# Kernel tuning notes

Hardware: AMD Instinct MI355X
Metric: run time of the kernel (lower is better)

The kernel has to match this reference:

```python
import jax, jax.numpy as jnp
import numpy as np

B, N, M, D = 8, 512, 64, 128
H = 64  # mlp_hidden_dim


def setup_inputs() -> dict:
    key = jax.random.key(0)
    ks = jax.random.split(key, 10)
    op_emb = jax.random.normal(ks[0], (B, N, D), dtype=jnp.float32)
    machine_emb = jax.random.normal(ks[1], (B, M, D), dtype=jnp.float32)
    edge_emb = jax.random.normal(ks[2], (B, N, M, D), dtype=jnp.float32)
    action_mask = jax.random.randint(ks[3], (B, N, M), 0, 2) > 0
    s1 = 1.0 / np.sqrt(3 * D)
    s2 = 1.0 / np.sqrt(H)
    W1 = jax.random.uniform(ks[4], (3 * D, H), jnp.float32, -s1, s1)
    b1 = jax.random.uniform(ks[5], (H,), jnp.float32, -s1, s1)
    W2 = jax.random.uniform(ks[6], (H, H), jnp.float32, -s2, s2)
    b2 = jax.random.uniform(ks[7], (H,), jnp.float32, -s2, s2)
    W3 = jax.random.uniform(ks[8], (H, 1), jnp.float32, -s2, s2)
    b3 = jax.random.uniform(ks[9], (1,), jnp.float32, -s2, s2)
    return {"op_emb": op_emb, "machine_emb": machine_emb, "edge_emb": edge_emb,
            "action_mask": action_mask,
            "W1": W1, "b1": b1, "W2": W2, "b2": b2, "W3": W3, "b3": b3}


def reference(op_emb, machine_emb, edge_emb, action_mask, W1, b1, W2, b2, W3, b3):
    # Split first linear over the three concat chunks to avoid materializing
    # the (B,N,M,3D) concat tensor (same math as cat -> Linear).
    Wo, Wm, We = W1[:D], W1[D:2 * D], W1[2 * D:]
    h = (jnp.einsum('bnd,dh->bnh', op_emb, Wo)[:, :, None, :]
         + jnp.einsum('bmd,dh->bmh', machine_emb, Wm)[:, None, :, :]
         + jnp.einsum('bnmd,dh->bnmh', edge_emb, We) + b1)  # (B,N,M,H)
    h = jax.nn.relu(h)
    h = jax.nn.relu(h @ W2 + b2)
    scores = (h @ W3 + b3)[..., 0]  # (B,N,M)
    scores = jnp.where(action_mask, scores, -jnp.inf)
    return jax.nn.log_softmax(scores.reshape(B, N * M), axis=-1)
```

## Files before the change

### kernel.cpp

```cpp
#include <hip/hip_runtime.h>
#include <math.h>

#define Bb 8
#define Nn 512
#define Mm 64
#define Dd 128
#define Hh 64
#define Gg 4
#define NEG_BIG (-1.0e30f)

typedef __bf16 bf16x8 __attribute__((ext_vector_type(8)));
typedef float  f32x4  __attribute__((ext_vector_type(4)));

#define WS_WEB   0u
#define WS_W2B   16384u
#define WS_CWS   24576u
#define WS_AOP   155648u
#define WS_SCORE 1204224u

__global__ __launch_bounds__(256) void wprep_kernel(
    const float* __restrict__ W1, const float* __restrict__ W2, char* __restrict__ ws)
{
    __bf16* WeB = (__bf16*)(ws + WS_WEB);
    __bf16* W2B = (__bf16*)(ws + WS_W2B);
    int idx = blockIdx.x * 256 + threadIdx.x;
    if (idx < 8192) {
        int fid = idx >> 9, rem = idx & 511;
        int lane = rem >> 3, j = rem & 7;
        int t = fid >> 2, ks = fid & 3;
        int q = lane >> 4, ln = lane & 15;
        int d = ks * 32 + q * 8 + j;
        int h = t * 16 + ln;
        WeB[idx] = (__bf16)W1[(size_t)(2 * Dd + d) * Hh + h];
    } else if (idx < 12288) {
        int i2 = idx - 8192;
        int fid = i2 >> 9, rem = i2 & 511;
        int lane = rem >> 3, j = rem & 7;
        int t = fid >> 1, ks = fid & 1;
        int q = lane >> 4, ln = lane & 15;
        int k = ks * 32 + q * 8 + j;
        int h = t * 16 + ln;
        W2B[i2] = (__bf16)W2[(size_t)k * Hh + h];
    }
}

__global__ __launch_bounds__(64) void proj_kernel(
    const float* __restrict__ op_emb, const float* __restrict__ machine_emb,
    const float* __restrict__ W1, const float* __restrict__ b1, char* __restrict__ ws)
{
    float* Cws = (float*)(ws + WS_CWS);
    float* Aop = (float*)(ws + WS_AOP);
    const int bid = blockIdx.x;
    const int h = threadIdx.x;
    if (bid < Bb * Mm) {
        const float* mg = machine_emb + (size_t)bid * Dd;
        const float* Wm = W1 + (size_t)Dd * Hh;
        float acc = b1[h];
#pragma unroll 8
        for (int d = 0; d < Dd; ++d) acc = fmaf(mg[d], Wm[d * Hh + h], acc);
        Cws[(size_t)bid * Hh + h] = acc;
    } else {
        const int bn = bid - Bb * Mm;
        const float* og = op_emb + (size_t)bn * Dd;
        float acc = 0.f;
#pragma unroll 8
        for (int d = 0; d < Dd; ++d) acc = fmaf(og[d], W1[d * Hh + h], acc);
        Aop[(size_t)bn * Hh + h] = acc;
    }
}

__global__ __launch_bounds__(256, 3) void main_kernel(
    const float* __restrict__ edge_emb, const int* __restrict__ mask,
    const float* __restrict__ b2, const float* __restrict__ W3,
    const float* __restrict__ b3, char* __restrict__ ws)
{
    __shared__ __bf16 sWeB[8192];
    __shared__ __bf16 sW2B[4096];
    __shared__ __bf16 sH1[Mm * 72];

    const float* Cws = (const float*)(ws + WS_CWS);
    const float* Aop = (const float*)(ws + WS_AOP);
    float* scores    = (float*)(ws + WS_SCORE);

    const int tid  = threadIdx.x;
    const int lane = tid & 63;
    const int w    = tid >> 6;
    const int q    = lane >> 4;
    const int ln   = lane & 15;
    const int bn0  = blockIdx.x * Gg;
    const int b    = bn0 >> 9;
    const int mrow = w * 16 + ln;

    {
        const float4* s1 = (const float4*)(ws + WS_WEB);
        float4* d1 = (float4*)sWeB;
        for (int i = tid; i < 1024; i += 256) d1[i] = s1[i];
        const float4* s2 = (const float4*)(ws + WS_W2B);
        float4* d2 = (float4*)sW2B;
        for (int i = tid; i < 512; i += 256) d2[i] = s2[i];
    }

    float cv[16];
#pragma unroll
    for (int t = 0; t < 4; ++t)
#pragma unroll
        for (int r = 0; r < 4; ++r)
            cv[t * 4 + r] = Cws[((size_t)b * Mm + w * 16 + q * 4 + r) * Hh + t * 16 + ln];
    float b2v[4], w3v[4];
#pragma unroll
    for (int t = 0; t < 4; ++t) { b2v[t] = b2[t * 16 + ln]; w3v[t] = W3[t * 16 + ln]; }
    const float bias3 = b3[0];

    float4 raw[8]; float aopv[4]; int4 mk = {0, 0, 0, 0};
    {
        const float* Eg = edge_emb + (size_t)bn0 * (Mm * Dd) + mrow * Dd + q * 8;
#pragma unroll
        for (int ks = 0; ks < 4; ++ks) {
            raw[2 * ks]     = *(const float4*)&Eg[ks * 32];
            raw[2 * ks + 1] = *(const float4*)&Eg[ks * 32 + 4];
        }
#pragma unroll
        for (int t = 0; t < 4; ++t) aopv[t] = Aop[(size_t)bn0 * Hh + t * 16 + ln];
        if (ln == 0) mk = *(const int4*)&mask[(size_t)bn0 * Mm + w * 16 + q * 4];
    }

    __syncthreads();

#pragma unroll
    for (int g = 0; g < Gg; ++g) {
        const int bn = bn0 + g;

        float4 nraw[8] = {};
        float  naop[4] = {};
        int4   nmk = {0, 0, 0, 0};
        if (g + 1 < Gg) {
            const float* Eg = edge_emb + (size_t)(bn + 1) * (Mm * Dd) + mrow * Dd + q * 8;
#pragma unroll
            for (int ks = 0; ks < 4; ++ks) {
                nraw[2 * ks]     = *(const float4*)&Eg[ks * 32];
                nraw[2 * ks + 1] = *(const float4*)&Eg[ks * 32 + 4];
            }
#pragma unroll
            for (int t = 0; t < 4; ++t) naop[t] = Aop[(size_t)(bn + 1) * Hh + t * 16 + ln];
            if (ln == 0) nmk = *(const int4*)&mask[(size_t)(bn + 1) * Mm + w * 16 + q * 4];
        }

        bf16x8 af[4];
#pragma unroll
        for (int ks = 0; ks < 4; ++ks) {
            float4 lo = raw[2 * ks], hi = raw[2 * ks + 1];
            bf16x8 a;
            a[0] = (__bf16)lo.x; a[1] = (__bf16)lo.y; a[2] = (__bf16)lo.z; a[3] = (__bf16)lo.w;
            a[4] = (__bf16)hi.x; a[5] = (__bf16)hi.y; a[6] = (__bf16)hi.z; a[7] = (__bf16)hi.w;
            af[ks] = a;
        }

        f32x4 acc[4];
#pragma unroll
        for (int t = 0; t < 4; ++t) acc[t] = (f32x4){0.f, 0.f, 0.f, 0.f};
#pragma unroll
        for (int t = 0; t < 4; ++t)
#pragma unroll
            for (int ks = 0; ks < 4; ++ks) {
                bf16x8 bfr = *(const bf16x8*)&sWeB[((t * 4 + ks) * 64 + lane) * 8];
                acc[t] = __builtin_amdgcn_mfma_f32_16x16x32_bf16(af[ks], bfr, acc[t], 0, 0, 0);
            }

#pragma unroll
        for (int t = 0; t < 4; ++t) {
            float av = aopv[t];
#pragma unroll
            for (int r = 0; r < 4; ++r) {
                float v = fmaxf(acc[t][r] + av + cv[t * 4 + r], 0.f);
                sH1[(w * 16 + q * 4 + r) * 72 + t * 16 + ln] = (__bf16)v;
            }
        }

        bf16x8 a2[2];
#pragma unroll
        for (int ks = 0; ks < 2; ++ks)
            a2[ks] = *(const bf16x8*)&sH1[(w * 16 + ln) * 72 + ks * 32 + q * 8];
        f32x4 c2[4];
#pragma unroll
        for (int t = 0; t < 4; ++t) c2[t] = (f32x4){0.f, 0.f, 0.f, 0.f};
#pragma unroll
        for (int t = 0; t < 4; ++t)
#pragma unroll
            for (int ks = 0; ks < 2; ++ks) {
                bf16x8 bfr = *(const bf16x8*)&sW2B[((t * 2 + ks) * 64 + lane) * 8];
                c2[t] = __builtin_amdgcn_mfma_f32_16x16x32_bf16(a2[ks], bfr, c2[t], 0, 0, 0);
            }

        float p[4] = {0.f, 0.f, 0.f, 0.f};
#pragma unroll
        for (int t = 0; t < 4; ++t)
#pragma unroll
            for (int r = 0; r < 4; ++r)
                p[r] += fmaxf(c2[t][r] + b2v[t], 0.f) * w3v[t];
#pragma unroll
        for (int r = 0; r < 4; ++r) {
            p[r] += __shfl_xor(p[r], 1, 64);
            p[r] += __shfl_xor(p[r], 2, 64);
            p[r] += __shfl_xor(p[r], 4, 64);
            p[r] += __shfl_xor(p[r], 8, 64);
        }
        if (ln == 0) {
            float4 o;
            o.x = mk.x ? (p[0] + bias3) : NEG_BIG;
            o.y = mk.y ? (p[1] + bias3) : NEG_BIG;
            o.z = mk.z ? (p[2] + bias3) : NEG_BIG;
            o.w = mk.w ? (p[3] + bias3) : NEG_BIG;
            *(float4*)&scores[(size_t)bn * Mm + w * 16 + q * 4] = o;
        }

#pragma unroll
        for (int i = 0; i < 8; ++i) raw[i] = nraw[i];
#pragma unroll
        for (int t = 0; t < 4; ++t) aopv[t] = naop[t];
        mk = nmk;
    }
}

__global__ __launch_bounds__(1024) void lsm_kernel(
    const char* __restrict__ ws, float* __restrict__ out)
{
    const float* s = (const float*)(ws + WS_SCORE) + (size_t)blockIdx.x * (Nn * Mm);
    __shared__ float redA[16];
    __shared__ float redB[16];
    const int tid = threadIdx.x;

    float lm = -INFINITY;
    for (int i = tid; i < Nn * Mm; i += 1024) lm = fmaxf(lm, s[i]);
#pragma unroll
    for (int off = 32; off > 0; off >>= 1) lm = fmaxf(lm, __shfl_xor(lm, off, 64));
    if ((tid & 63) == 0) redA[tid >> 6] = lm;
    __syncthreads();
    float gm = redA[0];
#pragma unroll
    for (int k = 1; k < 16; ++k) gm = fmaxf(gm, redA[k]);

    float ls = 0.f;
    for (int i = tid; i < Nn * Mm; i += 1024) ls += expf(s[i] - gm);
#pragma unroll
    for (int off = 32; off > 0; off >>= 1) ls += __shfl_xor(ls, off, 64);
    if ((tid & 63) == 0) redB[tid >> 6] = ls;
    __syncthreads();
    float gs = 0.f;
#pragma unroll
    for (int k = 0; k < 16; ++k) gs += redB[k];

    const float cc = gm + logf(gs);
    for (int i = tid; i < Nn * Mm; i += 1024)
        out[(size_t)blockIdx.x * (Nn * Mm) + i] = s[i] - cc;
}

extern "C" void kernel_launch(void* const* d_in, const int* in_sizes, int n_in,
                              void* d_out, int out_size, void* d_ws, size_t ws_size,
                              hipStream_t stream)
{
    const float* op_emb      = (const float*)d_in[0];
    const float* machine_emb = (const float*)d_in[1];
    const float* edge_emb    = (const float*)d_in[2];
    const int*   mask        = (const int*)  d_in[3];
    const float* W1 = (const float*)d_in[4];
    const float* b1 = (const float*)d_in[5];
    const float* W2 = (const float*)d_in[6];
    const float* b2 = (const float*)d_in[7];
    const float* W3 = (const float*)d_in[8];
    const float* b3 = (const float*)d_in[9];
    char* ws = (char*)d_ws;

    wprep_kernel<<<48, 256, 0, stream>>>(W1, W2, ws);
    proj_kernel<<<Bb * Mm + Bb * Nn, 64, 0, stream>>>(op_emb, machine_emb, W1, b1, ws);
    main_kernel<<<(Bb * Nn) / Gg, 256, 0, stream>>>(edge_emb, mask, b2, W3, b3, ws);
    lsm_kernel<<<Bb, 1024, 0, stream>>>(ws, (float*)d_out);
}
```

Measured before the change: 244.4 us.

## Split log-softmax into parallel partial, combine and apply kernels; stage biases in LDS

The single 8-block log-softmax kernel is replaced by three kernels: a 512-block pass that computes a per-chunk max and sum-exp, an 8-block combine, and a vectorised elementwise apply. This spreads the reduction across far more CUs than the old 8-block launch. The main kernel now stages the per-batch machine projection, op projection and mask in shared memory and seeds the MFMA accumulators with the bias sum. It also streamlines the prefetch registers. The cost is two extra kernel launches and more LDS per block, which may lower occupancy in the main kernel.

Result: faster. 238.5 us (-2.4%).

```diff
diff --git a/kernel.cpp b/kernel.cpp
--- a/kernel.cpp
+++ b/kernel.cpp
@@ -17,6 +17,8 @@
 #define WS_CWS   24576u
 #define WS_AOP   155648u
 #define WS_SCORE 1204224u
+#define WS_PART  2252800u
+#define WS_CC    2256896u
 
 __global__ __launch_bounds__(256) void wprep_kernel(
     const float* __restrict__ W1, const float* __restrict__ W2, char* __restrict__ ws)
@@ -76,11 +78,12 @@
 {
     __shared__ __bf16 sWeB[8192];
     __shared__ __bf16 sW2B[4096];
+    __shared__ float  sCws[Mm * Hh];
     __shared__ __bf16 sH1[Mm * 72];
-
-    const float* Cws = (const float*)(ws + WS_CWS);
-    const float* Aop = (const float*)(ws + WS_AOP);
-    float* scores    = (float*)(ws + WS_SCORE);
+    __shared__ float  sAop[Gg * Hh];
+    __shared__ int    sMask[Gg * Mm];
+
+    float* scores = (float*)(ws + WS_SCORE);
 
     const int tid  = threadIdx.x;
     const int lane = tid & 63;
@@ -98,30 +101,24 @@
         const float4* s2 = (const float4*)(ws + WS_W2B);
         float4* d2 = (float4*)sW2B;
         for (int i = tid; i < 512; i += 256) d2[i] = s2[i];
-    }
-
-    float cv[16];
-#pragma unroll
-    for (int t = 0; t < 4; ++t)
-#pragma unroll
-        for (int r = 0; r < 4; ++r)
-            cv[t * 4 + r] = Cws[((size_t)b * Mm + w * 16 + q * 4 + r) * Hh + t * 16 + ln];
+        const float4* s3 = (const float4*)(ws + WS_CWS) + (size_t)b * (Mm * Hh / 4);
+        float4* d3 = (float4*)sCws;
+        for (int i = tid; i < 1024; i += 256) d3[i] = s3[i];
+        sAop[tid] = ((const float*)(ws + WS_AOP))[(size_t)bn0 * Hh + tid];
+        sMask[tid] = mask[(size_t)bn0 * Mm + tid];
+    }
+
     float b2v[4], w3v[4];
 #pragma unroll
     for (int t = 0; t < 4; ++t) { b2v[t] = b2[t * 16 + ln]; w3v[t] = W3[t * 16 + ln]; }
     const float bias3 = b3[0];
 
-    float4 raw[8]; float aopv[4]; int4 mk = {0, 0, 0, 0};
-    {
-        const float* Eg = edge_emb + (size_t)bn0 * (Mm * Dd) + mrow * Dd + q * 8;
-#pragma unroll
-        for (int ks = 0; ks < 4; ++ks) {
-            raw[2 * ks]     = *(const float4*)&Eg[ks * 32];
-            raw[2 * ks + 1] = *(const float4*)&Eg[ks * 32 + 4];
-        }
-#pragma unroll
-        for (int t = 0; t < 4; ++t) aopv[t] = Aop[(size_t)bn0 * Hh + t * 16 + ln];
-        if (ln == 0) mk = *(const int4*)&mask[(size_t)bn0 * Mm + w * 16 + q * 4];
+    const float* Eg0 = edge_emb + (size_t)bn0 * (Mm * Dd) + mrow * Dd + q * 8;
+    float4 raw[8];
+#pragma unroll
+    for (int ks = 0; ks < 4; ++ks) {
+        raw[2 * ks]     = *(const float4*)&Eg0[ks * 32];
+        raw[2 * ks + 1] = *(const float4*)&Eg0[ks * 32 + 4];
     }
 
     __syncthreads();
@@ -129,21 +126,6 @@
 #pragma unroll
     for (int g = 0; g < Gg; ++g) {
         const int bn = bn0 + g;
-
-        float4 nraw[8] = {};
-        float  naop[4] = {};
-        int4   nmk = {0, 0, 0, 0};
-        if (g + 1 < Gg) {
-            const float* Eg = edge_emb + (size_t)(bn + 1) * (Mm * Dd) + mrow * Dd + q * 8;
-#pragma unroll
-            for (int ks = 0; ks < 4; ++ks) {
-                nraw[2 * ks]     = *(const float4*)&Eg[ks * 32];
-                nraw[2 * ks + 1] = *(const float4*)&Eg[ks * 32 + 4];
-            }
-#pragma unroll
-            for (int t = 0; t < 4; ++t) naop[t] = Aop[(size_t)(bn + 1) * Hh + t * 16 + ln];
-            if (ln == 0) nmk = *(const int4*)&mask[(size_t)(bn + 1) * Mm + w * 16 + q * 4];
-        }
 
         bf16x8 af[4];
 #pragma unroll
@@ -154,10 +136,24 @@
             a[4] = (__bf16)hi.x; a[5] = (__bf16)hi.y; a[6] = (__bf16)hi.z; a[7] = (__bf16)hi.w;
             af[ks] = a;
         }
+        if (g + 1 < Gg) {
+            const float* Eg = edge_emb + (size_t)(bn + 1) * (Mm * Dd) + mrow * Dd + q * 8;
+#pragma unroll
+            for (int ks = 0; ks < 4; ++ks) {
+                raw[2 * ks]     = *(const float4*)&Eg[ks * 32];
+                raw[2 * ks + 1] = *(const float4*)&Eg[ks * 32 + 4];
+            }
+        }
 
         f32x4 acc[4];
 #pragma unroll
-        for (int t = 0; t < 4; ++t) acc[t] = (f32x4){0.f, 0.f, 0.f, 0.f};
+        for (int t = 0; t < 4; ++t) {
+            float av = sAop[g * Hh + t * 16 + ln];
+#pragma unroll
+            for (int r = 0; r < 4; ++r)
+                acc[t][r] = av + sCws[(w * 16 + q * 4 + r) * Hh + t * 16 + ln];
+        }
+
 #pragma unroll
         for (int t = 0; t < 4; ++t)
 #pragma unroll
@@ -167,14 +163,11 @@
             }
 
 #pragma unroll
-        for (int t = 0; t < 4; ++t) {
-            float av = aopv[t];
-#pragma unroll
-            for (int r = 0; r < 4; ++r) {
-                float v = fmaxf(acc[t][r] + av + cv[t * 4 + r], 0.f);
-                sH1[(w * 16 + q * 4 + r) * 72 + t * 16 + ln] = (__bf16)v;
-            }
-        }
+        for (int t = 0; t < 4; ++t)
+#pragma unroll
+            for (int r = 0; r < 4; ++r)
+                sH1[(w * 16 + q * 4 + r) * 72 + t * 16 + ln] =
+                    (__bf16)fmaxf(acc[t][r], 0.f);
 
         bf16x8 a2[2];
 #pragma unroll
@@ -205,53 +198,70 @@
             p[r] += __shfl_xor(p[r], 8, 64);
         }
         if (ln == 0) {
+            int m0 = w * 16 + q * 4;
             float4 o;
-            o.x = mk.x ? (p[0] + bias3) : NEG_BIG;
-            o.y = mk.y ? (p[1] + bias3) : NEG_BIG;
-            o.z = mk.z ? (p[2] + bias3) : NEG_BIG;
-            o.w = mk.w ? (p[3] + bias3) : NEG_BIG;
-            *(float4*)&scores[(size_t)bn * Mm + w * 16 + q * 4] = o;
-        }
-
-#pragma unroll
-        for (int i = 0; i < 8; ++i) raw[i] = nraw[i];
-#pragma unroll
-        for (int t = 0; t < 4; ++t) aopv[t] = naop[t];
-        mk = nmk;
-    }
-}
-
-__global__ __launch_bounds__(1024) void lsm_kernel(
+            o.x = sMask[g * Mm + m0 + 0] ? (p[0] + bias3) : NEG_BIG;
+            o.y = sMask[g * Mm + m0 + 1] ? (p[1] + bias3) : NEG_BIG;
+            o.z = sMask[g * Mm + m0 + 2] ? (p[2] + bias3) : NEG_BIG;
+            o.w = sMask[g * Mm + m0 + 3] ? (p[3] + bias3) : NEG_BIG;
+            *(float4*)&scores[(size_t)bn * Mm + m0] = o;
+        }
+    }
+}
+
+__global__ __launch_bounds__(256) void lsm_part_kernel(char* __restrict__ ws)
+{
+    const float* s = (const float*)(ws + WS_SCORE);
+    float* part = (float*)(ws + WS_PART);
+    __shared__ float sm[4], ss[4];
+    const int c = blockIdx.x;
+    const int tid = threadIdx.x;
+    const int lane = tid & 63, wv = tid >> 6;
+
+    float2 v = *(const float2*)&s[(size_t)c * 512 + tid * 2];
+    float m = fmaxf(v.x, v.y);
+#pragma unroll
+    for (int off = 1; off < 64; off <<= 1) m = fmaxf(m, __shfl_xor(m, off, 64));
+    if (lane == 0) sm[wv] = m;
+    __syncthreads();
+    float gm = fmaxf(fmaxf(sm[0], sm[1]), fmaxf(sm[2], sm[3]));
+
+    float e = expf(v.x - gm) + expf(v.y - gm);
+#pragma unroll
+    for (int off = 1; off < 64; off <<= 1) e += __shfl_xor(e, off, 64);
+    if (lane == 0) ss[wv] = e;
+    __syncthreads();
+    if (tid == 0) {
+        float2 o; o.x = gm; o.y = ss[0] + ss[1] + ss[2] + ss[3];
+        *(float2*)&part[c * 2] = o;
+    }
+}
+
+__global__ __launch_bounds__(64) void lsm_comb_kernel(char* __restrict__ ws)
+{
+    const float* part = (const float*)(ws + WS_PART);
+    float* cc = (float*)(ws + WS_CC);
+    const int b = blockIdx.x, t = threadIdx.x;
+    float2 p = *(const float2*)&part[(b * 64 + t) * 2];
+    float gm = p.x;
+#pragma unroll
+    for (int off = 1; off < 64; off <<= 1) gm = fmaxf(gm, __shfl_xor(gm, off, 64));
+    float l = p.y * expf(p.x - gm);
+#pragma unroll
+    for (int off = 1; off < 64; off <<= 1) l += __shfl_xor(l, off, 64);
+    if (t == 0) cc[b] = gm + logf(l);
+}
+
+__global__ __launch_bounds__(256) void lsm_apply_kernel(
     const char* __restrict__ ws, float* __restrict__ out)
 {
-    const float* s = (const float*)(ws + WS_SCORE) + (size_t)blockIdx.x * (Nn * Mm);
-    __shared__ float redA[16];
-    __shared__ float redB[16];
-    const int tid = threadIdx.x;
-
-    float lm = -INFINITY;
-    for (int i = tid; i < Nn * Mm; i += 1024) lm = fmaxf(lm, s[i]);
-#pragma unroll
-    for (int off = 32; off > 0; off >>= 1) lm = fmaxf(lm, __shfl_xor(lm, off, 64));
-    if ((tid & 63) == 0) redA[tid >> 6] = lm;
-    __syncthreads();
-    float gm = redA[0];
-#pragma unroll
-    for (int k = 1; k < 16; ++k) gm = fmaxf(gm, redA[k]);
-
-    float ls = 0.f;
-    for (int i = tid; i < Nn * Mm; i += 1024) ls += expf(s[i] - gm);
-#pragma unroll
-    for (int off = 32; off > 0; off >>= 1) ls += __shfl_xor(ls, off, 64);
-    if ((tid & 63) == 0) redB[tid >> 6] = ls;
-    __syncthreads();
-    float gs = 0.f;
-#pragma unroll
-    for (int k = 0; k < 16; ++k) gs += redB[k];
-
-    const float cc = gm + logf(gs);
-    for (int i = tid; i < Nn * Mm; i += 1024)
-        out[(size_t)blockIdx.x * (Nn * Mm) + i] = s[i] - cc;
+    const float4* s4 = (const float4*)(ws + WS_SCORE);
+    const float* cc = (const float*)(ws + WS_CC);
+    const int i = blockIdx.x * 256 + threadIdx.x;
+    const float c = cc[i >> 13];
+    float4 v = s4[i];
+    v.x -= c; v.y -= c; v.z -= c; v.w -= c;
+    ((float4*)out)[i] = v;
 }
 
 extern "C" void kernel_launch(void* const* d_in, const int* in_sizes, int n_in,
@@ -273,5 +283,7 @@
     wprep_kernel<<<48, 256, 0, stream>>>(W1, W2, ws);
     proj_kernel<<<Bb * Mm + Bb * Nn, 64, 0, stream>>>(op_emb, machine_emb, W1, b1, ws);
     main_kernel<<<(Bb * Nn) / Gg, 256, 0, stream>>>(edge_emb, mask, b2, W3, b3, ws);
-    lsm_kernel<<<Bb, 1024, 0, stream>>>(ws, (float*)d_out);
-}
+    lsm_part_kernel<<<512, 256, 0, stream>>>(ws);
+    lsm_comb_kernel<<<Bb, 64, 0, stream>>>(ws);
+    lsm_apply_kernel<<<256, 256, 0, stream>>>(ws, (float*)d_out);
+}
```
